# Kernel optimization log

Measured on AMD Instinct MI355X. Metric: run time of the kernel, lower is better.

The kernel has to match this reference:

```python
import jax, jax.numpy as jnp
import numpy as np

DN = ('NCH', 'OIH', 'NCH')

def conv1d(x, w, b, pad):
    y = jax.lax.conv_general_dilated(x, w, (1,), [(pad, pad)], dimension_numbers=DN)
    return y if b is None else y + b[None, :, None]

def bn_eval(x, g, b, m, v, eps):
    s = g * jax.lax.rsqrt(v + eps)
    return x * s[None, :, None] + (b - m * s)[None, :, None]

def swish(x):
    return x * jax.nn.sigmoid(x)

def setup_inputs() -> dict:
    key = jax.random.key(0)
    ks = jax.random.split(key, 8)
    B, T, P = 16, 8192, 32
    inp = {
        'x': jax.random.normal(ks[0], (B, 1, T), jnp.float32),
        'conv_w': jax.random.normal(ks[1], (512, 1, 9), jnp.float32) * 0.1,
        'bn_g': jnp.ones((512,), jnp.float32),
        'bn_b': jnp.zeros((512,), jnp.float32),
        'bn_m': jnp.zeros((512,), jnp.float32),
        'bn_v': jnp.ones((512,), jnp.float32),
        'p1_w': jax.random.normal(ks[2], (P, 2, 31), jnp.float32) * 0.1,
        'p1_b': jnp.zeros((P,), jnp.float32),
        'pbn1_g': jnp.ones((P,), jnp.float32),
        'pbn1_b': jnp.zeros((P,), jnp.float32),
        'pbn1_m': jnp.zeros((P,), jnp.float32),
        'pbn1_v': jnp.ones((P,), jnp.float32),
        'p2_w': jax.random.normal(ks[3], (P, P, 15), jnp.float32) * 0.05,
        'p2_b': jnp.zeros((P,), jnp.float32),
        'pbn2_g': jnp.ones((P,), jnp.float32),
        'pbn2_b': jnp.zeros((P,), jnp.float32),
        'pbn2_m': jnp.zeros((P,), jnp.float32),
        'pbn2_v': jnp.ones((P,), jnp.float32),
        'p3_w': jax.random.normal(ks[4], (2, P, 15), jnp.float32) * 0.001,  # source scales last conv weight by 0.01
        'p3_b': jnp.full((2,), -np.log(2.0), jnp.float32),                 # source sets bias to -log(2)
        'norm_mean': jnp.ones((1,), jnp.float32),                           # eval-mode renorm buffer
    }
    return inp

def reference(x, conv_w, bn_g, bn_b, bn_m, bn_v,
              p1_w, p1_b, pbn1_g, pbn1_b, pbn1_m, pbn1_v,
              p2_w, p2_b, pbn2_g, pbn2_b, pbn2_m, pbn2_v,
              p3_w, p3_b, norm_mean):
    B, _, T = x.shape
    # main conv -> BN(eps=1e-3) -> GLU(dim=1); dropout is identity in eval
    h = conv1d(x, conv_w, None, 9 // 2)                 # [B, 512, T]
    h = bn_eval(h, bn_g, bn_b, bn_m, bn_v, 1e-3)
    a, g = jnp.split(h, 2, axis=1)
    features = a * jax.nn.sigmoid(g)                    # [B, 256, T]
    # predictor on cat([x, x*x])
    j = conv1d(jnp.concatenate([x, x * x], axis=1), p1_w, p1_b, 15)
    j = swish(bn_eval(j, pbn1_g, pbn1_b, pbn1_m, pbn1_v, 1e-5))
    j = conv1d(j, p2_w, p2_b, 7)
    j = swish(bn_eval(j, pbn2_g, pbn2_b, pbn2_m, pbn2_v, 1e-5))
    j = conv1d(j, p3_w, p3_b, 7)                        # [B, 2, T]
    weights = jax.nn.sigmoid(j[:, 0, :])                # [B, T]
    moves = jax.nn.sigmoid(j[:, 1, :])
    bmoves = moves
    moves = moves * norm_mean[0]                        # eval: renorm = norm_mean buffer
    # CIF-style dynamic pooling (row_pool), vectorized over batch
    feats = jnp.transpose(features, (0, 2, 1))          # [B, T, C]
    fw = feats * weights[..., None]
    poses = jnp.cumsum(jax.lax.stop_gradient(moves), axis=1)  # moves.detach() in source
    floors = jnp.floor(poses)
    w1 = 1.0 - (poses - floors)
    w2 = poses - floors
    fl = floors.astype(jnp.int32)
    ce = fl + 1
    Lmax = T + 2  # static bound: poses <= T so ceil index <= T+1
    C = fw.shape[2]
    def pool(fw_i, fl_i, ce_i, w1_i, w2_i):
        out = jnp.zeros((Lmax, C), fw_i.dtype)
        out = out.at[fl_i].add(w1_i[:, None] * fw_i)
        out = out.at[ce_i].add(w2_i[:, None] * fw_i)
        return out
    x_evs = jax.vmap(pool)(fw, fl, ce, w1, w2)          # [B, Lmax, C]
    lens = fl[:, -1] + 2                                 # int(ceils[-1]) + 1
    x_evs = jnp.transpose(x_evs, (0, 2, 1))             # [B, C, Lmax]
    pad = 3 - (Lmax % 3)
    x_evs = jnp.pad(x_evs, ((0, 0), (0, 0), (0, pad)))
    return x_evs, lens, bmoves, weights
```

## Files before the change

### kernel.cpp

```cpp
#include <hip/hip_runtime.h>
#include <math.h>

static constexpr int TT = 8192;
static constexpr int LFULL = 8196;
static constexpr int BSTRIDE = LFULL + 2;

static constexpr size_t XE_OFF   = 0;
static constexpr size_t LENS_OFF = (size_t)16*256*LFULL;
static constexpr size_t BM_OFF   = LENS_OFF + 16;
static constexpr size_t WT_OFF   = BM_OFF + (size_t)16*TT;

static constexpr size_t U_OFF     = 0;
static constexpr size_t V_OFF     = U_OFF + (size_t)16*32*TT;
static constexpr size_t MOVES_OFF = V_OFF + (size_t)16*32*TT;
static constexpr size_t C1_OFF    = MOVES_OFF + (size_t)16*TT;
static constexpr size_t C2_OFF    = C1_OFF + (size_t)16*TT;
static constexpr size_t BND_OFF   = U_OFF;

__device__ __forceinline__ float sig_(float z) { return 1.0f / (1.0f + __expf(-z)); }

__global__ __launch_bounds__(256) void k_conv1(
    const float* __restrict__ x,
    const float* __restrict__ p1w, const float* __restrict__ p1b,
    const float* __restrict__ g1, const float* __restrict__ b1,
    const float* __restrict__ m1, const float* __restrict__ v1,
    float* __restrict__ u)
{
    __shared__ float xin[2 * 320];
    __shared__ float w1t[2 * 992];
    const int tid = threadIdx.x;
    const int b = blockIdx.y;
    const int t0 = blockIdx.x * 256;

    for (int idx = tid; idx < 640; idx += 256) {
        int ci = idx / 320, xl = idx - ci * 320;
        int id = t0 - 15 + xl;
        float val = 0.f;
        if (xl < 286 && id >= 0 && id < TT) val = x[b * TT + id];
        xin[idx] = ci ? val * val : val;
    }
    for (int idx = tid; idx < 1984; idx += 256) {
        int c = idx / 62; int r = idx - c * 62; int ci = r / 31; int k = r - ci * 31;
        w1t[ci * 992 + c * 31 + k] = p1w[idx];
    }
    __syncthreads();

    const int tg = tid >> 5, c = tid & 31;
    float acc[32];
    const float bias = p1b[c];
#pragma unroll
    for (int i = 0; i < 32; ++i) acc[i] = bias;

    for (int h = 0; h < 4; ++h) {
        for (int ci = 0; ci < 2; ++ci) {
            float win[40];
            const float4* wp = (const float4*)(&xin[ci * 320 + tg * 32 + h * 8]);
#pragma unroll
            for (int r = 0; r < 10; ++r) {
                float4 q = wp[r];
                win[4*r] = q.x; win[4*r+1] = q.y; win[4*r+2] = q.z; win[4*r+3] = q.w;
            }
#pragma unroll
            for (int k = 0; k < 31; ++k) {
                float w = w1t[ci * 992 + c * 31 + k];
#pragma unroll
                for (int i = 0; i < 8; ++i) acc[h*8+i] = fmaf(w, win[i + k], acc[h*8+i]);
            }
        }
    }
    const float s = g1[c] * rsqrtf(v1[c] + 1e-5f);
    const float sh = b1[c] - m1[c] * s;
    float* up = &u[((size_t)(b * 32 + c)) * TT + t0 + tg * 32];
#pragma unroll
    for (int i = 0; i < 8; ++i) {
        float z0 = fmaf(acc[4*i+0], s, sh);
        float z1 = fmaf(acc[4*i+1], s, sh);
        float z2 = fmaf(acc[4*i+2], s, sh);
        float z3 = fmaf(acc[4*i+3], s, sh);
        ((float4*)up)[i] = make_float4(z0 * sig_(z0), z1 * sig_(z1), z2 * sig_(z2), z3 * sig_(z3));
    }
}

__global__ __launch_bounds__(256) void k_conv2(
    const float* __restrict__ u,
    const float* __restrict__ p2w, const float* __restrict__ p2b,
    const float* __restrict__ g2, const float* __restrict__ b2,
    const float* __restrict__ m2, const float* __restrict__ v2,
    float* __restrict__ vout)
{
    __shared__ float uld[16 * 272];
    __shared__ float w2t[16 * 256];
    const int tid = threadIdx.x;
    const int b = blockIdx.y;
    const int t0 = blockIdx.x * 256;
    const int ch = blockIdx.z;

    const int tg = tid >> 4, cl = tid & 15;
    const int c = ch * 16 + cl;
    float acc[16];
    const float bias = p2b[c];
#pragma unroll
    for (int i = 0; i < 16; ++i) acc[i] = bias;

    for (int h = 0; h < 2; ++h) {
        __syncthreads();
        for (int idx = tid; idx < 16 * 272; idx += 256) {
            int ci = idx >> 8; int tl = idx & 255;
            ci = idx / 272; tl = idx - ci * 272;
            int tgl = t0 - 7 + tl;
            float val = 0.f;
            if (tl < 270 && tgl >= 0 && tgl < TT) val = u[((size_t)(b * 32 + h * 16 + ci)) * TT + tgl];
            uld[idx] = val;
        }
        for (int idx = tid; idx < 16 * 256; idx += 256) {
            int ci = idx >> 8; int r = idx & 255; int cl2 = r >> 4; int k = r & 15;
            w2t[idx] = (k < 15) ? p2w[(ch * 16 + cl2) * 480 + (h * 16 + ci) * 15 + k] : 0.f;
        }
        __syncthreads();

        for (int ci = 0; ci < 16; ++ci) {
            float win[32];
            const float4* wp = (const float4*)(&uld[ci * 272 + tg * 16]);
#pragma unroll
            for (int r = 0; r < 8; ++r) {
                float4 q = wp[r];
                win[4*r] = q.x; win[4*r+1] = q.y; win[4*r+2] = q.z; win[4*r+3] = q.w;
            }
            float w[16];
            const float4* wqp = (const float4*)(&w2t[ci * 256 + cl * 16]);
#pragma unroll
            for (int r = 0; r < 4; ++r) {
                float4 q = wqp[r];
                w[4*r] = q.x; w[4*r+1] = q.y; w[4*r+2] = q.z; w[4*r+3] = q.w;
            }
#pragma unroll
            for (int k = 0; k < 15; ++k) {
#pragma unroll
                for (int i = 0; i < 16; ++i) acc[i] = fmaf(w[k], win[i + k], acc[i]);
            }
        }
    }
    const float s = g2[c] * rsqrtf(v2[c] + 1e-5f);
    const float sh = b2[c] - m2[c] * s;
    float o[16];
#pragma unroll
    for (int i = 0; i < 16; ++i) { float z = fmaf(acc[i], s, sh); o[i] = z * sig_(z); }
    float* vp = &vout[((size_t)(b * 32 + c)) * TT + t0 + tg * 16];
#pragma unroll
    for (int r = 0; r < 4; ++r)
        ((float4*)vp)[r] = make_float4(o[4*r], o[4*r+1], o[4*r+2], o[4*r+3]);
}

__global__ __launch_bounds__(256) void k_conv3(
    const float* __restrict__ vin,
    const float* __restrict__ p3w, const float* __restrict__ p3b,
    const float* __restrict__ nm,
    float* __restrict__ outw, float* __restrict__ outbm, float* __restrict__ moves)
{
    __shared__ float vld[32 * 272];
    const int tid = threadIdx.x;
    const int b = blockIdx.y;
    const int t0 = blockIdx.x * 256;

    for (int idx = tid; idx < 32 * 272; idx += 256) {
        int ci = idx / 272, tl = idx - ci * 272;
        int tg = t0 - 7 + tl;
        float val = 0.f;
        if (tl < 270 && tg >= 0 && tg < TT) val = vin[((size_t)(b * 32 + ci)) * TT + tg];
        vld[idx] = val;
    }
    __syncthreads();

    float a0 = p3b[0], a1 = p3b[1];
    for (int ci = 0; ci < 32; ++ci) {
        float win[15];
#pragma unroll
        for (int k = 0; k < 15; ++k) win[k] = vld[ci * 272 + tid + k];
#pragma unroll
        for (int k = 0; k < 15; ++k) {
            a0 = fmaf(p3w[ci * 15 + k], win[k], a0);
            a1 = fmaf(p3w[480 + ci * 15 + k], win[k], a1);
        }
    }
    const int t = t0 + tid;
    const float wt = sig_(a0);
    const float bm = sig_(a1);
    outw[b * TT + t] = wt;
    outbm[b * TT + t] = bm;
    moves[b * TT + t] = bm * nm[0];
}

__global__ __launch_bounds__(1024) void k_scan(
    const float* __restrict__ moves, const float* __restrict__ wts,
    float* __restrict__ coef1, float* __restrict__ coef2,
    int* __restrict__ bnd, float* __restrict__ lens)
{
    __shared__ float wsum[16];
    const int tid = threadIdx.x;
    const int b = blockIdx.x;
    const int lane = tid & 63, wv = tid >> 6;
    float carry = 0.f;

    int* bb = &bnd[b * BSTRIDE];
    for (int i = tid; i < BSTRIDE; i += 1024) bb[i] = TT;
    if (tid == 0) { bb[0] = 0; bb[1] = 0; }
    __syncthreads();

    const float4* mv4 = (const float4*)&moves[b * TT];
    const float4* wt4 = (const float4*)&wts[b * TT];
    float4* c14 = (float4*)&coef1[b * TT];
    float4* c24 = (float4*)&coef2[b * TT];

    for (int chunk = 0; chunk < 2; ++chunk) {
        const int idx = chunk * 1024 + tid;
        float4 m = mv4[idx];
        const float s = m.x + m.y + m.z + m.w;
        float v = s;
#pragma unroll
        for (int off = 1; off < 64; off <<= 1) {
            float n = __shfl_up(v, off, 64);
            if (lane >= off) v += n;
        }
        if (lane == 63) wsum[wv] = v;
        __syncthreads();
        float pre = carry;
        for (int w = 0; w < wv; ++w) pre += wsum[w];
        float tot = 0.f;
#pragma unroll
        for (int w = 0; w < 16; ++w) tot += wsum[w];
        const float base = pre + (v - s);
        const float p0 = base + m.x;
        const float p1 = p0 + m.y;
        const float p2 = p1 + m.z;
        const float p3 = p2 + m.w;
        const float4 w4 = wt4[idx];
        const float fr0 = p0 - floorf(p0), fr1 = p1 - floorf(p1);
        const float fr2 = p2 - floorf(p2), fr3 = p3 - floorf(p3);
        c14[idx] = make_float4((1.f - fr0) * w4.x, (1.f - fr1) * w4.y,
                               (1.f - fr2) * w4.z, (1.f - fr3) * w4.w);
        c24[idx] = make_float4(fr0 * w4.x, fr1 * w4.y, fr2 * w4.z, fr3 * w4.w);
        {
            int lf = (int)floorf(base) + 1;
            const int lfe = (int)floorf(p3);
            const int tbase = idx << 2;
            for (; lf <= lfe; ++lf) {
                const float lff = (float)lf;
                int t = tbase;
                if (p0 >= lff) { }
                else if (p1 >= lff) t += 1;
                else if (p2 >= lff) t += 2;
                else t += 3;
                if (lf + 1 < BSTRIDE) bb[lf + 1] = t;
            }
        }
        if (chunk == 1 && tid == 1023) lens[b] = floorf(p3) + 2.0f;
        carry += tot;
        __syncthreads();
    }
}

__global__ __launch_bounds__(256) void k_zero(
    const float* __restrict__ lens, float* __restrict__ xevs)
{
    const int b = blockIdx.y;
    const int cg = blockIdx.x;
    const int zs = (((int)lens[b]) + 15) & ~15;
    if (zs >= LFULL) return;
    const int n4 = (LFULL - zs) >> 2;
    const float4 z = make_float4(0.f, 0.f, 0.f, 0.f);
    for (int r = 0; r < 4; ++r) {
        float4* row4 = (float4*)&xevs[((size_t)(b * 256 + cg * 4 + r)) * LFULL + zs];
        for (int i = threadIdx.x; i < n4; i += 256) row4[i] = z;
    }
}

static constexpr int LTILE = 32;
static constexpr int CHK = 128;

__global__ __launch_bounds__(256) void k_pool(
    const float* __restrict__ x,
    const float* __restrict__ cw,
    const float* __restrict__ bng, const float* __restrict__ bnb,
    const float* __restrict__ bnm, const float* __restrict__ bnv,
    const float* __restrict__ coef1, const float* __restrict__ coef2,
    const int* __restrict__ bnd,
    float* __restrict__ xevs)
{
    __shared__ float out_lds[256 * 33];
    __shared__ float4 xl4[36];
    __shared__ float4 c1l4[CHK / 4], c2l4[CHK / 4];
    __shared__ int lbs[LTILE + 2];
    float* xl = (float*)xl4;
    float* c1l = (float*)c1l4;
    float* c2l = (float*)c2l4;

    const int tid = threadIdx.x;
    const int b = blockIdx.y;
    const int l0 = blockIdx.x * LTILE;
    const int LTa = min(LTILE, LFULL - l0);

    if (tid < LTa + 2) lbs[tid] = bnd[b * BSTRIDE + l0 + tid];
    __syncthreads();

    const int t_lo = lbs[0];
    const int t_hi = lbs[LTa + 1];
    if (t_lo >= t_hi) return;

    const size_t rowbase = (size_t)b * 256 * LFULL + l0;

#pragma unroll
    for (int li = 0; li < 33; ++li) out_lds[tid * 33 + li] = 0.f;

    const int c = tid;
    float wa[9], wg[9];
#pragma unroll
    for (int k = 0; k < 9; ++k) { wa[k] = cw[c * 9 + k]; wg[k] = cw[(c + 256) * 9 + k]; }
    const float sa = bng[c] * rsqrtf(bnv[c] + 1e-3f);
    const float sha = bnb[c] - bnm[c] * sa;
    const float sg = bng[c + 256] * rsqrtf(bnv[c + 256] + 1e-3f);
    const float shg = bnb[c + 256] - bnm[c + 256] * sg;

    const float* xg = &x[b * TT];
    const float* c1g = &coef1[b * TT];
    const float* c2g = &coef2[b * TT];

    float accA = 0.f, accB = 0.f;
    int j = 0;
    int nb = lbs[1];

    for (int cs = t_lo; cs < t_hi; cs += CHK) {
        const int ce = min(cs + CHK, t_hi);
        const int len = ce - cs;
        __syncthreads();
        for (int idx = tid; idx < len + 12; idx += 256) {
            int id = cs - 4 + idx;
            xl[idx] = (id >= 0 && id < TT) ? xg[id] : 0.f;
        }
        if (tid < len) { c1l[tid] = c1g[cs + tid]; c2l[tid] = c2g[cs + tid]; }
        __syncthreads();

        const int len4 = len >> 2;
        for (int g = 0; g < len4; ++g) {
            float4 A = xl4[g], Bq = xl4[g + 1], Cq = xl4[g + 2];
            float w[12] = {A.x, A.y, A.z, A.w, Bq.x, Bq.y, Bq.z, Bq.w, Cq.x, Cq.y, Cq.z, Cq.w};
            float f[4];
#pragma unroll
            for (int i = 0; i < 4; ++i) {
                float s0 = 0.f, s1 = 0.f;
#pragma unroll
                for (int k = 0; k < 9; ++k) { s0 = fmaf(wa[k], w[i + k], s0); s1 = fmaf(wg[k], w[i + k], s1); }
                const float av = fmaf(s0, sa, sha);
                const float gv = fmaf(s1, sg, shg);
                f[i] = av * sig_(gv);
            }
            float4 c1v = c1l4[g], c2v = c2l4[g];
            const float c1a[4] = {c1v.x, c1v.y, c1v.z, c1v.w};
            const float c2a[4] = {c2v.x, c2v.y, c2v.z, c2v.w};
            const int tb = cs + (g << 2);
#pragma unroll
            for (int i = 0; i < 4; ++i) {
                const int t = tb + i;
                while (t >= nb) {
                    int li = j - 1;
                    if (li >= 0 && li < LTa) out_lds[c * 33 + li] = accA;
                    accA = accB; accB = 0.f;
                    ++j;
                    nb = lbs[j + 1];
                }
                accA = fmaf(c1a[i], f[i], accA);
                accB = fmaf(c2a[i], f[i], accB);
            }
        }
        for (int t = cs + (len4 << 2); t < ce; ++t) {
            const int il = t - cs;
            float s0 = 0.f, s1 = 0.f;
#pragma unroll
            for (int k = 0; k < 9; ++k) { float xv = xl[il + k]; s0 = fmaf(wa[k], xv, s0); s1 = fmaf(wg[k], xv, s1); }
            const float av = fmaf(s0, sa, sha);
            const float gv = fmaf(s1, sg, shg);
            const float f0 = av * sig_(gv);
            while (t >= nb) {
                int li = j - 1;
                if (li >= 0 && li < LTa) out_lds[c * 33 + li] = accA;
                accA = accB; accB = 0.f;
                ++j;
                nb = lbs[j + 1];
            }
            accA = fmaf(c1l[il], f0, accA);
            accB = fmaf(c2l[il], f0, accB);
        }
    }
    {
        int li = j - 1;
        if (li >= 0 && li < LTa) out_lds[c * 33 + li] = accA;
    }
    __syncthreads();

#pragma unroll
    for (int it = 0; it < 8; ++it) {
        int idx4 = it * 256 + tid;
        int cc = idx4 >> 3, q = (idx4 & 7) << 2;
        if (q < LTa) {
            float4 o;
            o.x = out_lds[cc * 33 + q + 0];
            o.y = out_lds[cc * 33 + q + 1];
            o.z = out_lds[cc * 33 + q + 2];
            o.w = out_lds[cc * 33 + q + 3];
            *(float4*)(&xevs[rowbase + (size_t)cc * LFULL + q]) = o;
        }
    }
}

extern "C" void kernel_launch(void* const* d_in, const int* in_sizes, int n_in,
                              void* d_out, int out_size, void* d_ws, size_t ws_size,
                              hipStream_t stream) {
    (void)in_sizes; (void)n_in; (void)out_size; (void)ws_size;
    const float* x      = (const float*)d_in[0];
    const float* conv_w = (const float*)d_in[1];
    const float* bn_g   = (const float*)d_in[2];
    const float* bn_b   = (const float*)d_in[3];
    const float* bn_m   = (const float*)d_in[4];
    const float* bn_v   = (const float*)d_in[5];
    const float* p1_w   = (const float*)d_in[6];
    const float* p1_b   = (const float*)d_in[7];
    const float* pbn1_g = (const float*)d_in[8];
    const float* pbn1_b = (const float*)d_in[9];
    const float* pbn1_m = (const float*)d_in[10];
    const float* pbn1_v = (const float*)d_in[11];
    const float* p2_w   = (const float*)d_in[12];
    const float* p2_b   = (const float*)d_in[13];
    const float* pbn2_g = (const float*)d_in[14];
    const float* pbn2_b = (const float*)d_in[15];
    const float* pbn2_m = (const float*)d_in[16];
    const float* pbn2_v = (const float*)d_in[17];
    const float* p3_w   = (const float*)d_in[18];
    const float* p3_b   = (const float*)d_in[19];
    const float* nm     = (const float*)d_in[20];

    float* out = (float*)d_out;
    float* ws  = (float*)d_ws;
    float* u     = ws + U_OFF;
    float* v     = ws + V_OFF;
    float* moves = ws + MOVES_OFF;
    float* coef1 = ws + C1_OFF;
    float* coef2 = ws + C2_OFF;
    int*   bnd   = (int*)(ws + BND_OFF);
    float* xevs  = out + XE_OFF;
    float* lens  = out + LENS_OFF;
    float* bmv   = out + BM_OFF;
    float* wts   = out + WT_OFF;

    k_conv1<<<dim3(32, 16), 256, 0, stream>>>(x, p1_w, p1_b, pbn1_g, pbn1_b, pbn1_m, pbn1_v, u);
    k_conv2<<<dim3(32, 16, 2), 256, 0, stream>>>(u, p2_w, p2_b, pbn2_g, pbn2_b, pbn2_m, pbn2_v, v);
    k_conv3<<<dim3(32, 16), 256, 0, stream>>>(v, p3_w, p3_b, nm, wts, bmv, moves);
    k_scan<<<16, 1024, 0, stream>>>(moves, wts, coef1, coef2, bnd, lens);
    k_zero<<<dim3(64, 16), 256, 0, stream>>>(lens, xevs);
    k_pool<<<dim3((LFULL + LTILE - 1) / LTILE, 16), 256, 0, stream>>>(
        x, conv_w, bn_g, bn_b, bn_m, bn_v, coef1, coef2, bnd, xevs);
}
```

Before: 355.9 us.

## Register-tile conv3 with LDS weights and merge zero-fill into pool kernel

k_conv3 now gives each thread four output timesteps and a quarter of the input channels. Weights are staged in shared memory, windows are loaded with padded float4 LDS reads, and partial sums are reduced with shuffles. The separate k_zero launch is folded into k_pool as extra blocks, which removes one kernel launch. The pool chunk size CHK doubles to 256, enlarging the staging buffers. The aim is to cut launch overhead and the scalar LDS and global weight loads in conv3, at the cost of more shared memory per pool block.

```diff
diff --git a/kernel.cpp b/kernel.cpp
--- a/kernel.cpp
+++ b/kernel.cpp
@@ -105,8 +105,7 @@
     for (int h = 0; h < 2; ++h) {
         __syncthreads();
         for (int idx = tid; idx < 16 * 272; idx += 256) {
-            int ci = idx >> 8; int tl = idx & 255;
-            ci = idx / 272; tl = idx - ci * 272;
+            int ci = idx / 272, tl = idx - ci * 272;
             int tgl = t0 - 7 + tl;
             float val = 0.f;
             if (tl < 270 && tgl >= 0 && tgl < TT) val = u[((size_t)(b * 32 + h * 16 + ci)) * TT + tgl];
@@ -157,7 +156,8 @@
     const float* __restrict__ nm,
     float* __restrict__ outw, float* __restrict__ outbm, float* __restrict__ moves)
 {
-    __shared__ float vld[32 * 272];
+    __shared__ float vld[32 * 276];
+    __shared__ float wsh[960];
     const int tid = threadIdx.x;
     const int b = blockIdx.y;
     const int t0 = blockIdx.x * 256;
@@ -167,27 +167,55 @@
         int tg = t0 - 7 + tl;
         float val = 0.f;
         if (tl < 270 && tg >= 0 && tg < TT) val = vin[((size_t)(b * 32 + ci)) * TT + tg];
-        vld[idx] = val;
-    }
+        vld[ci * 276 + tl] = val;
+    }
+    for (int idx = tid; idx < 960; idx += 256) wsh[idx] = p3w[idx];
     __syncthreads();
 
-    float a0 = p3b[0], a1 = p3b[1];
-    for (int ci = 0; ci < 32; ++ci) {
-        float win[15];
-#pragma unroll
-        for (int k = 0; k < 15; ++k) win[k] = vld[ci * 272 + tid + k];
+    const int g = tid >> 2;
+    const int q = tid & 3;
+    float acc[8];
+#pragma unroll
+    for (int i = 0; i < 8; ++i) acc[i] = 0.f;
+
+#pragma unroll
+    for (int i = 0; i < 8; ++i) {
+        const int ci = q + 4 * i;
+        float win[20];
+        const float4* wp = (const float4*)(&vld[ci * 276 + g * 4]);
+#pragma unroll
+        for (int r = 0; r < 5; ++r) {
+            float4 v4 = wp[r];
+            win[4*r] = v4.x; win[4*r+1] = v4.y; win[4*r+2] = v4.z; win[4*r+3] = v4.w;
+        }
+        const float* w0 = &wsh[ci * 15];
+        const float* w1 = &wsh[480 + ci * 15];
 #pragma unroll
         for (int k = 0; k < 15; ++k) {
-            a0 = fmaf(p3w[ci * 15 + k], win[k], a0);
-            a1 = fmaf(p3w[480 + ci * 15 + k], win[k], a1);
-        }
-    }
-    const int t = t0 + tid;
-    const float wt = sig_(a0);
-    const float bm = sig_(a1);
-    outw[b * TT + t] = wt;
-    outbm[b * TT + t] = bm;
-    moves[b * TT + t] = bm * nm[0];
+            const float a = w0[k], gw = w1[k];
+#pragma unroll
+            for (int tt = 0; tt < 4; ++tt) {
+                acc[tt]     = fmaf(a,  win[k + tt], acc[tt]);
+                acc[4 + tt] = fmaf(gw, win[k + tt], acc[4 + tt]);
+            }
+        }
+    }
+#pragma unroll
+    for (int i = 0; i < 8; ++i) {
+        acc[i] += __shfl_xor(acc[i], 1, 64);
+        acc[i] += __shfl_xor(acc[i], 2, 64);
+    }
+    if (q == 0) {
+        const float nmv = nm[0];
+        const float b0 = p3b[0], b1 = p3b[1];
+        const int t = t0 + g * 4;
+        float4 wv = make_float4(sig_(acc[0]+b0), sig_(acc[1]+b0), sig_(acc[2]+b0), sig_(acc[3]+b0));
+        float4 bm = make_float4(sig_(acc[4]+b1), sig_(acc[5]+b1), sig_(acc[6]+b1), sig_(acc[7]+b1));
+        float4 mv = make_float4(bm.x*nmv, bm.y*nmv, bm.z*nmv, bm.w*nmv);
+        *(float4*)&outw[b * TT + t]  = wv;
+        *(float4*)&outbm[b * TT + t] = bm;
+        *(float4*)&moves[b * TT + t] = mv;
+    }
 }
 
 __global__ __launch_bounds__(1024) void k_scan(
@@ -259,23 +287,9 @@
     }
 }
 
-__global__ __launch_bounds__(256) void k_zero(
-    const float* __restrict__ lens, float* __restrict__ xevs)
-{
-    const int b = blockIdx.y;
-    const int cg = blockIdx.x;
-    const int zs = (((int)lens[b]) + 15) & ~15;
-    if (zs >= LFULL) return;
-    const int n4 = (LFULL - zs) >> 2;
-    const float4 z = make_float4(0.f, 0.f, 0.f, 0.f);
-    for (int r = 0; r < 4; ++r) {
-        float4* row4 = (float4*)&xevs[((size_t)(b * 256 + cg * 4 + r)) * LFULL + zs];
-        for (int i = threadIdx.x; i < n4; i += 256) row4[i] = z;
-    }
-}
-
 static constexpr int LTILE = 32;
-static constexpr int CHK = 128;
+static constexpr int CHK = 256;
+static constexpr int NPOOLX = (LFULL + LTILE - 1) / LTILE;
 
 __global__ __launch_bounds__(256) void k_pool(
     const float* __restrict__ x,
@@ -283,11 +297,11 @@
     const float* __restrict__ bng, const float* __restrict__ bnb,
     const float* __restrict__ bnm, const float* __restrict__ bnv,
     const float* __restrict__ coef1, const float* __restrict__ coef2,
-    const int* __restrict__ bnd,
+    const int* __restrict__ bnd, const float* __restrict__ lens,
     float* __restrict__ xevs)
 {
     __shared__ float out_lds[256 * 33];
-    __shared__ float4 xl4[36];
+    __shared__ float4 xl4[68];
     __shared__ float4 c1l4[CHK / 4], c2l4[CHK / 4];
     __shared__ int lbs[LTILE + 2];
     float* xl = (float*)xl4;
@@ -296,6 +310,20 @@
 
     const int tid = threadIdx.x;
     const int b = blockIdx.y;
+
+    if (blockIdx.x >= NPOOLX) {
+        const int zx = blockIdx.x - NPOOLX;
+        const int zs = (((int)lens[b]) + 15) & ~15;
+        if (zs >= LFULL) return;
+        const int n4 = (LFULL - zs) >> 2;
+        const float4 z = make_float4(0.f, 0.f, 0.f, 0.f);
+        for (int r = 0; r < 4; ++r) {
+            float4* row4 = (float4*)&xevs[((size_t)(b * 256 + zx * 4 + r)) * LFULL + zs];
+            for (int i = tid; i < n4; i += 256) row4[i] = z;
+        }
+        return;
+    }
+
     const int l0 = blockIdx.x * LTILE;
     const int LTa = min(LTILE, LFULL - l0);
 
@@ -454,7 +482,6 @@
     k_conv2<<<dim3(32, 16, 2), 256, 0, stream>>>(u, p2_w, p2_b, pbn2_g, pbn2_b, pbn2_m, pbn2_v, v);
     k_conv3<<<dim3(32, 16), 256, 0, stream>>>(v, p3_w, p3_b, nm, wts, bmv, moves);
     k_scan<<<16, 1024, 0, stream>>>(moves, wts, coef1, coef2, bnd, lens);
-    k_zero<<<dim3(64, 16), 256, 0, stream>>>(lens, xevs);
-    k_pool<<<dim3((LFULL + LTILE - 1) / LTILE, 16), 256, 0, stream>>>(
-        x, conv_w, bn_g, bn_b, bn_m, bn_v, coef1, coef2, bnd, xevs);
-}
+    k_pool<<<dim3(NPOOLX + 64, 16), 256, 0, stream>>>(
+        x, conv_w, bn_g, bn_b, bn_m, bn_v, coef1, coef2, bnd, lens, xevs);
+}
```

Result: faster. 339.4 us (-4.6%).
